# Optimization experiments

Hardware: AMD Instinct MI355X
Metric: run time of the kernel (lower is better)

## Reference

```python
import jax, jax.numpy as jnp
import numpy as np

B, SEQ, HORIZON, NKEYS = 256, 512, 32, 8192
L1, HIDDEN, L2 = 64, 128, 64


def _lstm_layer(x, Wih, Whh, bih, bhh):
    # x: [B, T, IN]; PyTorch gate order i, f, g, o
    Bn, T, _ = x.shape
    H = Whh.shape[1]
    xT = jnp.transpose(x, (1, 0, 2))  # [T, B, IN]
    pre_x = jnp.einsum('tbi,gi->tbg', xT, Wih) + bih + bhh  # precompute input part

    def step(carry, px):
        h, c = carry
        gates = px + h @ Whh.T
        i, f, g, o = jnp.split(gates, 4, axis=-1)
        i = jax.nn.sigmoid(i); f = jax.nn.sigmoid(f)
        g = jnp.tanh(g); o = jax.nn.sigmoid(o)
        c = f * c + i * g
        h = o * jnp.tanh(c)
        return (h, c), h

    h0 = jnp.zeros((Bn, H), x.dtype)
    c0 = jnp.zeros((Bn, H), x.dtype)
    _, hs = jax.lax.scan(step, (h0, c0), pre_x)
    return jnp.transpose(hs, (1, 0, 2))  # [B, T, H]


def setup_inputs():
    key = jax.random.key(0)
    ks = jax.random.split(key, 20)
    s = 0.05
    inp = jax.random.normal(ks[0], (B, SEQ), jnp.float32)
    akey = jax.random.normal(ks[1], (NKEYS, SEQ), jnp.float32)
    aval = jax.random.normal(ks[2], (NKEYS, SEQ + HORIZON), jnp.float32)
    W1 = jax.random.normal(ks[3], (L1, HORIZON + 1), jnp.float32) * s
    b1 = jnp.zeros((L1,), jnp.float32)
    Wih0 = jax.random.normal(ks[4], (4 * HIDDEN, L1), jnp.float32) * s
    Whh0 = jax.random.normal(ks[5], (4 * HIDDEN, HIDDEN), jnp.float32) * s
    bih0 = jnp.zeros((4 * HIDDEN,), jnp.float32)
    bhh0 = jnp.zeros((4 * HIDDEN,), jnp.float32)
    Wih1 = jax.random.normal(ks[6], (4 * HIDDEN, HIDDEN), jnp.float32) * s
    Whh1 = jax.random.normal(ks[7], (4 * HIDDEN, HIDDEN), jnp.float32) * s
    bih1 = jnp.zeros((4 * HIDDEN,), jnp.float32)
    bhh1 = jnp.zeros((4 * HIDDEN,), jnp.float32)
    W2 = jax.random.normal(ks[8], (L2, HIDDEN), jnp.float32) * s
    b2 = jnp.zeros((L2,), jnp.float32)
    W3 = jax.random.normal(ks[9], (HORIZON, L2), jnp.float32) * s
    b3 = jnp.zeros((HORIZON,), jnp.float32)
    return {"input": inp, "attention_key": akey, "attention_value": aval,
            "W1": W1, "b1": b1,
            "Wih0": Wih0, "Whh0": Whh0, "bih0": bih0, "bhh0": bhh0,
            "Wih1": Wih1, "Whh1": Whh1, "bih1": bih1, "bhh1": bhh1,
            "W2": W2, "b2": b2, "W3": W3, "b3": b3}


def reference(input, attention_key, attention_value, W1, b1,
              Wih0, Whh0, bih0, bhh0, Wih1, Whh1, bih1, bhh1,
              W2, b2, W3, b3):
    Bn = input.shape[0]
    # masked distance softmax attention: zero out per-row argmax before softmax
    distance = input @ attention_key.T  # [B, NKEYS]
    max_idx = jnp.argmax(distance, axis=1)
    distance = distance.at[jnp.arange(Bn), max_idx].set(0.0)
    a = jax.nn.softmax(distance, axis=1)
    hist = a @ attention_value  # [B, SEQ + HORIZON]
    # vectorized sliding-window unfold: [B, SEQ, HORIZON]
    win = jnp.arange(SEQ)[:, None] + jnp.arange(HORIZON)[None, :]
    ref_feats = hist[:, win]
    x = jnp.concatenate([input[:, :, None], ref_feats], axis=2)  # [B, SEQ, HORIZON+1]
    x = jnp.tanh(x @ W1.T + b1)  # [B, SEQ, L1]
    h = _lstm_layer(x, Wih0, Whh0, bih0, bhh0)
    h = _lstm_layer(h, Wih1, Whh1, bih1, bhh1)
    h = jnp.tanh(h)
    last = h[:, -1, :]  # [B, HIDDEN]
    l2 = jnp.tanh(last @ W2.T + b2)
    return l2 @ W3.T + b3  # [B, HORIZON]
```

## Files before the change

kernel.cpp:

```cpp
#include <hip/hip_runtime.h>

typedef _Float16 h8 __attribute__((ext_vector_type(8)));
typedef _Float16 h4 __attribute__((ext_vector_type(4)));
typedef float f32x4 __attribute__((ext_vector_type(4)));

__device__ __forceinline__ float fsigm(float x) {
    return __builtin_amdgcn_rcpf(1.0f + __expf(-x));
}
__device__ __forceinline__ float ftanh(float x) {
    return 1.0f - 2.0f * __builtin_amdgcn_rcpf(1.0f + __expf(2.0f * x));
}
__device__ __forceinline__ float fexp2(float x) {
    return __builtin_amdgcn_exp2f(x);
}
__device__ __forceinline__ void lds_barrier() {
    asm volatile("s_waitcnt lgkmcnt(0)\n\ts_barrier" ::: "memory");
}

#define L2E  1.4426950408889634f
#define L2E2 2.8853900817779268f

__global__ __launch_bounds__(256) void k_distM(const float* __restrict__ A,
                                               const float* __restrict__ Bm,
                                               float* __restrict__ C) {
    __shared__ _Float16 Ah[64][40], Al[64][40];
    __shared__ _Float16 Bh[64][40], Bl[64][40];
    const int n0 = blockIdx.x * 64;
    const int m0 = blockIdx.y * 64;
    const int tid = threadIdx.x;
    const int lane = tid & 63, wv = tid >> 6;
    const int quad = lane >> 4, l15 = lane & 15;
    f32x4 acc[4];
#pragma unroll
    for (int i = 0; i < 4; ++i) acc[i] = (f32x4){0.f, 0.f, 0.f, 0.f};

    int sm_[2], skq_[2];
    size_t arow[2], brow[2];
#pragma unroll
    for (int r = 0; r < 2; ++r) {
        int idx = tid + 256 * r;
        sm_[r] = idx >> 3; skq_[r] = (idx & 7) * 4;
        arow[r] = (size_t)(m0 + sm_[r]) * 512 + skq_[r];
        brow[r] = (size_t)(n0 + sm_[r]) * 512 + skq_[r];
    }
    float4 va[2], vb[2];
#pragma unroll
    for (int r = 0; r < 2; ++r) {
        va[r] = *(const float4*)&A[arow[r]];
        vb[r] = *(const float4*)&Bm[brow[r]];
    }

    for (int kt = 0; kt < 512; kt += 32) {
        lds_barrier();
#pragma unroll
        for (int r = 0; r < 2; ++r) {
            float e[4] = {va[r].x, va[r].y, va[r].z, va[r].w};
            h4 hi, lo;
#pragma unroll
            for (int j = 0; j < 4; ++j) {
                _Float16 h = (_Float16)e[j];
                hi[j] = h; lo[j] = (_Float16)(e[j] - (float)h);
            }
            *(h4*)&Ah[sm_[r]][skq_[r]] = hi;
            *(h4*)&Al[sm_[r]][skq_[r]] = lo;
            float f[4] = {vb[r].x, vb[r].y, vb[r].z, vb[r].w};
#pragma unroll
            for (int j = 0; j < 4; ++j) {
                _Float16 h = (_Float16)f[j];
                hi[j] = h; lo[j] = (_Float16)(f[j] - (float)h);
            }
            *(h4*)&Bh[sm_[r]][skq_[r]] = hi;
            *(h4*)&Bl[sm_[r]][skq_[r]] = lo;
        }
        lds_barrier();
        if (kt + 32 < 512) {
#pragma unroll
            for (int r = 0; r < 2; ++r) {
                va[r] = *(const float4*)&A[arow[r] + kt + 32];
                vb[r] = *(const float4*)&Bm[brow[r] + kt + 32];
            }
        }
        h8 ah = *(const h8*)&Ah[wv * 16 + l15][quad * 8];
        h8 al = *(const h8*)&Al[wv * 16 + l15][quad * 8];
#pragma unroll
        for (int nt = 0; nt < 4; ++nt) {
            h8 bhf = *(const h8*)&Bh[nt * 16 + l15][quad * 8];
            h8 blf = *(const h8*)&Bl[nt * 16 + l15][quad * 8];
            acc[nt] = __builtin_amdgcn_mfma_f32_16x16x32_f16(ah, bhf, acc[nt], 0, 0, 0);
            acc[nt] = __builtin_amdgcn_mfma_f32_16x16x32_f16(al, bhf, acc[nt], 0, 0, 0);
            acc[nt] = __builtin_amdgcn_mfma_f32_16x16x32_f16(ah, blf, acc[nt], 0, 0, 0);
        }
    }
#pragma unroll
    for (int nt = 0; nt < 4; ++nt)
#pragma unroll
        for (int r = 0; r < 4; ++r)
            C[(size_t)(m0 + wv * 16 + quad * 4 + r) * 8192 + n0 + nt * 16 + l15] = acc[nt][r];
}

__global__ __launch_bounds__(512) void k_softmax(float* __restrict__ D) {
    __shared__ float row[8192];
    __shared__ float r1[512];
    __shared__ int   ri[512];
    __shared__ float r2[512];
    const int b = blockIdx.x, tid = threadIdx.x;
    float* dr = D + (size_t)b * 8192;
    for (int i = tid; i < 2048; i += 512)
        *(float4*)&row[i * 4] = *(const float4*)&dr[i * 4];
    __syncthreads();

    float m1 = -INFINITY, m2 = -INFINITY; int i1 = 0x7fffffff;
    for (int i = tid; i < 8192; i += 512) {
        float v = row[i];
        if (v > m1) { m2 = m1; m1 = v; i1 = i; }
        else        { m2 = fmaxf(m2, v); }
    }
    r1[tid] = m1; ri[tid] = i1; r2[tid] = m2;
    __syncthreads();
    for (int s = 256; s > 0; s >>= 1) {
        if (tid < s) {
            float am1 = r1[tid], bm1 = r1[tid + s];
            int   ai1 = ri[tid], bi1 = ri[tid + s];
            float am2 = r2[tid], bm2 = r2[tid + s];
            bool bwins = (bm1 > am1) || (bm1 == am1 && bi1 < ai1);
            float wm1 = bwins ? bm1 : am1;
            int   wi1 = bwins ? bi1 : ai1;
            float lm1 = bwins ? am1 : bm1;
            float wm2 = fmaxf(fmaxf(am2, bm2), lm1);
            r1[tid] = wm1; ri[tid] = wi1; r2[tid] = wm2;
        }
        __syncthreads();
    }
    const int   I1 = ri[0];
    const float M  = fmaxf(r2[0], 0.0f);
    __syncthreads();

    float ssum = 0.0f;
    for (int i = tid; i < 8192; i += 512) {
        float v = (i == I1) ? 0.0f : row[i];
        float e = __expf(v - M);
        row[i] = e;
        ssum += e;
    }
    r1[tid] = ssum;
    __syncthreads();
    for (int s = 256; s > 0; s >>= 1) {
        if (tid < s) r1[tid] += r1[tid + s];
        __syncthreads();
    }
    const float inv = 1.0f / r1[0];
    for (int i = tid; i < 2048; i += 512) {
        float4 v = *(float4*)&row[i * 4];
        v.x *= inv; v.y *= inv; v.z *= inv; v.w *= inv;
        *(float4*)&dr[i * 4] = v;
    }
}

__global__ __launch_bounds__(256) void k_histM(const float* __restrict__ A,
                                               const float* __restrict__ Bm,
                                               float* __restrict__ C) {
    __shared__ _Float16 Ah[64][40], Al[64][40];
    __shared__ _Float16 Bh[64][40], Bl[64][40];
    const int n0 = blockIdx.x * 64;
    const int m0 = blockIdx.y * 64;
    const int kz = blockIdx.z;
    const int tid = threadIdx.x;
    const int lane = tid & 63, wv = tid >> 6;
    const int quad = lane >> 4, l15 = lane & 15;
    const int bn = tid & 63;
    const int ko = (tid >> 6) * 8;
    const bool bok = (n0 + bn) < 544;
    f32x4 acc[4];
#pragma unroll
    for (int i = 0; i < 4; ++i) acc[i] = (f32x4){0.f, 0.f, 0.f, 0.f};

    const int k_lo = kz * 512, k_hi = k_lo + 512;
    for (int kt = k_lo; kt < k_hi; kt += 32) {
        __syncthreads();
#pragma unroll
        for (int r = 0; r < 2; ++r) {
            int idx = tid + 256 * r;
            int m = idx >> 3, kq = (idx & 7) * 4;
            float4 v = *(const float4*)&A[(size_t)(m0 + m) * 8192 + kt + kq];
            float e[4] = {v.x, v.y, v.z, v.w};
            h4 hi, lo;
#pragma unroll
            for (int j = 0; j < 4; ++j) {
                _Float16 h = (_Float16)e[j];
                hi[j] = h; lo[j] = (_Float16)(e[j] - (float)h);
            }
            *(h4*)&Ah[m][kq] = hi;
            *(h4*)&Al[m][kq] = lo;
        }
        {
            float e[8];
#pragma unroll
            for (int j = 0; j < 8; ++j)
                e[j] = bok ? Bm[(size_t)(kt + ko + j) * 544 + n0 + bn] : 0.f;
            h8 hi, lo;
#pragma unroll
            for (int j = 0; j < 8; ++j) {
                _Float16 h = (_Float16)e[j];
                hi[j] = h; lo[j] = (_Float16)(e[j] - (float)h);
            }
            *(h8*)&Bh[bn][ko] = hi;
            *(h8*)&Bl[bn][ko] = lo;
        }
        __syncthreads();
        h8 ah = *(const h8*)&Ah[wv * 16 + l15][quad * 8];
        h8 al = *(const h8*)&Al[wv * 16 + l15][quad * 8];
#pragma unroll
        for (int nt = 0; nt < 4; ++nt) {
            h8 bhf = *(const h8*)&Bh[nt * 16 + l15][quad * 8];
            h8 blf = *(const h8*)&Bl[nt * 16 + l15][quad * 8];
            acc[nt] = __builtin_amdgcn_mfma_f32_16x16x32_f16(ah, bhf, acc[nt], 0, 0, 0);
            acc[nt] = __builtin_amdgcn_mfma_f32_16x16x32_f16(al, bhf, acc[nt], 0, 0, 0);
            acc[nt] = __builtin_amdgcn_mfma_f32_16x16x32_f16(ah, blf, acc[nt], 0, 0, 0);
        }
    }
#pragma unroll
    for (int nt = 0; nt < 4; ++nt)
#pragma unroll
        for (int r = 0; r < 4; ++r) {
            int n = n0 + nt * 16 + l15;
            if (n < 544)
                atomicAdd(&C[(size_t)(m0 + wv * 16 + quad * 4 + r) * 544 + n], acc[nt][r]);
        }
}

__global__ __launch_bounds__(256) void k_xfeat(const float* __restrict__ inp,
                                               const float* __restrict__ hist,
                                               const float* __restrict__ W1,
                                               const float* __restrict__ b1,
                                               float* __restrict__ X) {
    __shared__ float w[33 * 64];
    __shared__ float bl[64];
    __shared__ float il[128];
    __shared__ float hl[160];
    const int t0 = blockIdx.x * 128;
    const int b  = blockIdx.y;
    const int tid = threadIdx.x;
    for (int idx = tid; idx < 2112; idx += 256) {
        int o = idx / 33, k = idx % 33;
        w[k * 64 + o] = W1[idx];
    }
    if (tid < 64) bl[tid] = b1[tid];
    if (tid < 128) il[tid] = inp[(size_t)b * 512 + t0 + tid];
    for (int i = tid; i < 159; i += 256) hl[i] = hist[(size_t)b * 544 + t0 + i];
    __syncthreads();
    const int o = tid & 63, tq = tid >> 6;
    for (int it = 0; it < 32; ++it) {
        int tl = it * 4 + tq;
        float acc = fmaf(il[tl], w[o], bl[o]);
#pragma unroll
        for (int j = 0; j < 32; ++j)
            acc = fmaf(hl[tl + j], w[(1 + j) * 64 + o], acc);
        X[(size_t)(b * 512 + t0 + tl) * 64 + o] = ftanh(acc);
    }
}

template <int K>
__device__ __forceinline__ void pregemm_mfma(const float* __restrict__ A,
                                             const float* __restrict__ Bw,
                                             const float* __restrict__ bih,
                                             const float* __restrict__ bhh,
                                             float* __restrict__ C,
                                             int t0, int tcs, int gb, float* sm) {
    _Float16* Ah = (_Float16*)sm;
    _Float16* Al = Ah + 128 * 40;
    _Float16* Bh = Al + 128 * 40;
    _Float16* Bl = Bh + 128 * 40;
    const int n0 = (gb & 3) * 128;
    const int m0 = (gb >> 2) * 128;
    const int tid = threadIdx.x;
    const int lane = tid & 63, wv = tid >> 6;
    const int quad = lane >> 4, l15 = lane & 15;
    const int tcm = (1 << tcs) - 1;
    const int lr0 = tid >> 3, lr1 = lr0 + 64;
    const int kq  = (tid & 7) * 4;
    const int gr0 = m0 + lr0, gr1 = m0 + lr1;
    const size_t ar0 = ((size_t)(gr0 >> tcs) * 512 + t0 + (gr0 & tcm)) * K;
    const size_t ar1 = ((size_t)(gr1 >> tcs) * 512 + t0 + (gr1 & tcm)) * K;
    const size_t br0 = (size_t)(n0 + lr0) * K;
    const size_t br1 = (size_t)(n0 + lr1) * K;
    const float sb0 = (((n0 + lr0) >> 7) == 2) ? L2E2 : L2E;
    const float sb1 = (((n0 + lr1) >> 7) == 2) ? L2E2 : L2E;

    f32x4 acc[8];
#pragma unroll
    for (int i = 0; i < 8; ++i) acc[i] = (f32x4){0.f, 0.f, 0.f, 0.f};

    float4 va0 = *(const float4*)&A[ar0 + kq];
    float4 va1 = *(const float4*)&A[ar1 + kq];
    float4 vb0 = *(const float4*)&Bw[br0 + kq];
    float4 vb1 = *(const float4*)&Bw[br1 + kq];

    for (int kt = 0; kt < K; kt += 32) {
        lds_barrier();
        {
            float e[4]; h4 hi, lo;
            e[0] = va0.x; e[1] = va0.y; e[2] = va0.z; e[3] = va0.w;
#pragma unroll
            for (int j = 0; j < 4; ++j) {
                _Float16 h = (_Float16)e[j];
                hi[j] = h; lo[j] = (_Float16)(e[j] - (float)h);
            }
            *(h4*)&Ah[lr0 * 40 + kq] = hi; *(h4*)&Al[lr0 * 40 + kq] = lo;
            e[0] = va1.x; e[1] = va1.y; e[2] = va1.z; e[3] = va1.w;
#pragma unroll
            for (int j = 0; j < 4; ++j) {
                _Float16 h = (_Float16)e[j];
                hi[j] = h; lo[j] = (_Float16)(e[j] - (float)h);
            }
            *(h4*)&Ah[lr1 * 40 + kq] = hi; *(h4*)&Al[lr1 * 40 + kq] = lo;
            e[0] = vb0.x * sb0; e[1] = vb0.y * sb0; e[2] = vb0.z * sb0; e[3] = vb0.w * sb0;
#pragma unroll
            for (int j = 0; j < 4; ++j) {
                _Float16 h = (_Float16)e[j];
                hi[j] = h; lo[j] = (_Float16)(e[j] - (float)h);
            }
            *(h4*)&Bh[lr0 * 40 + kq] = hi; *(h4*)&Bl[lr0 * 40 + kq] = lo;
            e[0] = vb1.x * sb1; e[1] = vb1.y * sb1; e[2] = vb1.z * sb1; e[3] = vb1.w * sb1;
#pragma unroll
            for (int j = 0; j < 4; ++j) {
                _Float16 h = (_Float16)e[j];
                hi[j] = h; lo[j] = (_Float16)(e[j] - (float)h);
            }
            *(h4*)&Bh[lr1 * 40 + kq] = hi; *(h4*)&Bl[lr1 * 40 + kq] = lo;
        }
        lds_barrier();
        if (kt + 32 < K) {
            va0 = *(const float4*)&A[ar0 + kt + 32 + kq];
            va1 = *(const float4*)&A[ar1 + kt + 32 + kq];
            vb0 = *(const float4*)&Bw[br0 + kt + 32 + kq];
            vb1 = *(const float4*)&Bw[br1 + kt + 32 + kq];
        }
        h8 ah = *(const h8*)&Ah[(wv * 16 + l15) * 40 + quad * 8];
        h8 al = *(const h8*)&Al[(wv * 16 + l15) * 40 + quad * 8];
#pragma unroll
        for (int nt = 0; nt < 8; ++nt) {
            h8 bhf = *(const h8*)&Bh[(nt * 16 + l15) * 40 + quad * 8];
            h8 blf = *(const h8*)&Bl[(nt * 16 + l15) * 40 + quad * 8];
            acc[nt] = __builtin_amdgcn_mfma_f32_16x16x32_f16(ah, bhf, acc[nt], 0, 0, 0);
            acc[nt] = __builtin_amdgcn_mfma_f32_16x16x32_f16(al, bhf, acc[nt], 0, 0, 0);
            acc[nt] = __builtin_amdgcn_mfma_f32_16x16x32_f16(ah, blf, acc[nt], 0, 0, 0);
        }
    }
#pragma unroll
    for (int nt = 0; nt < 8; ++nt) {
        const int n = n0 + nt * 16 + l15;
        const float sc = ((n >> 7) == 2) ? L2E2 : L2E;
        const float bb = (bih[n] + bhh[n]) * sc;
#pragma unroll
        for (int r = 0; r < 4; ++r)
            C[(size_t)(m0 + wv * 16 + quad * 4 + r) * 512 + n] = acc[nt][r] + bb;
    }
}

__device__ __forceinline__ _Float16* hpl(float* sm, int buf, int b) {
    return (_Float16*)sm + ((buf * 16 + b) * 136);
}

template <int PH>
__device__ __forceinline__ void rec_step(
        float* sm,
        const h8 (&wh)[4][4],
        f32x4 (&pcs)[4][4],
        const float*& pp,
        float*& hob, bool wr, bool last,
        float (&c)[4],
        float* __restrict__ Sh, float* __restrict__ Sc,
        int l15, int quad, int un) {
    constexpr int RB = PH & 1;
    const _Float16* hp = hpl(sm, RB, l15);
    h8 hf[4];
#pragma unroll
    for (int q = 0; q < 4; ++q)
        hf[q] = *(const h8*)&hp[q * 32 + quad * 8];

    f32x4 aH[4];
#pragma unroll
    for (int g = 0; g < 4; ++g)
        aH[g] = __builtin_amdgcn_mfma_f32_16x16x32_f16(wh[g][0], hf[0], pcs[PH][g], 0, 0, 0);
#pragma unroll
    for (int g = 0; g < 4; ++g)
        pcs[PH][g] = *(const f32x4*)(pp + g * 128);
    pp += 512;
#pragma unroll
    for (int q = 1; q < 4; ++q)
#pragma unroll
        for (int g = 0; g < 4; ++g)
            aH[g] = __builtin_amdgcn_mfma_f32_16x16x32_f16(wh[g][q], hf[q], aH[g], 0, 0, 0);

    f32x4 hv;
#pragma unroll
    for (int r = 0; r < 4; ++r) {
        float A = fexp2(-aH[0][r]);
        float B = fexp2(-aH[1][r]);
        float Cv = fexp2(aH[2][r]);
        float D = fexp2(-aH[3][r]);
        float fv = __builtin_amdgcn_rcpf(1.0f + B);
        float ig = (Cv - 1.0f) *
                   __builtin_amdgcn_rcpf((1.0f + Cv) * (1.0f + A));
        c[r] = fmaf(c[r], fv, ig);
        float E = fexp2(c[r] * L2E2);
        hv[r] = (E - 1.0f) *
                __builtin_amdgcn_rcpf((1.0f + E) * (1.0f + D));
    }
    h4 hh;
#pragma unroll
    for (int j = 0; j < 4; ++j) hh[j] = (_Float16)hv[j];
    *(h4*)&hpl(sm, 1 - RB, l15)[un] = hh;
    if (wr) {
        *(f32x4*)hob = hv;
        hob += 128;
    }
    if (last) {
        *(f32x4*)Sh = hv;
        f32x4 cv = {c[0], c[1], c[2], c[3]};
        *(f32x4*)Sc = cv;
    }
    lds_barrier();
}

__device__ __forceinline__ void rec_body(const float* __restrict__ P,
                                         const float* __restrict__ Whh,
                                         float* __restrict__ S,
                                         float* __restrict__ Hout,
                                         int t0, int TC, int blk, float* sm) {
    const int b0   = blk * 16;
    const int tid  = threadIdx.x;
    const int lane = tid & 63;
    const int wv   = tid >> 6;
    const int quad = lane >> 4;
    const int l15  = lane & 15;
    const int un   = wv * 16 + quad * 4;
    const int nrow = wv * 16 + l15;

    h8 wh[4][4];
    const float gs[4] = {L2E, L2E, L2E2, L2E};
#pragma unroll
    for (int g = 0; g < 4; ++g) {
        const float sc = gs[g];
        int n = g * 128 + nrow;
#pragma unroll
        for (int q = 0; q < 4; ++q) {
            int kb = q * 32 + quad * 8;
            const float* wp = &Whh[(size_t)n * 128 + kb];
            float4 w0 = *(const float4*)wp;
            float4 w1 = *(const float4*)(wp + 4);
            float we[8] = {w0.x, w0.y, w0.z, w0.w, w1.x, w1.y, w1.z, w1.w};
#pragma unroll
            for (int j = 0; j < 8; ++j)
                wh[g][q][j] = (_Float16)(we[j] * sc);
        }
    }

    float* Sh = S + (size_t)(b0 + l15) * 128 + un;
    float* Sc = Sh + 32768;
    float4 h0 = *(const float4*)Sh;
    float4 c0 = *(const float4*)Sc;
    float c[4] = {c0.x, c0.y, c0.z, c0.w};
    {
        h4 hh;
        hh[0] = (_Float16)h0.x; hh[1] = (_Float16)h0.y;
        hh[2] = (_Float16)h0.z; hh[3] = (_Float16)h0.w;
        *(h4*)&hpl(sm, 0, l15)[un] = hh;
    }

    const bool wr = (Hout != nullptr);
    float* hob = wr ? (Hout + ((size_t)(b0 + l15) * 512 + t0) * 128 + un) : nullptr;

    const float* pp = P + (size_t)(b0 + l15) * TC * 512 + un;
    f32x4 pcs[4][4];
#pragma unroll
    for (int ph = 0; ph < 4; ++ph)
#pragma unroll
        for (int g = 0; g < 4; ++g)
            pcs[ph][g] = *(const f32x4*)(pp + ph * 512 + g * 128);
    pp += 4 * 512;

    lds_barrier();

    for (int tl = 0; tl < TC; tl += 4) {
        rec_step<0>(sm, wh, pcs, pp, hob, wr, false, c, Sh, Sc, l15, quad, un);
        rec_step<1>(sm, wh, pcs, pp, hob, wr, false, c, Sh, Sc, l15, quad, un);
        rec_step<2>(sm, wh, pcs, pp, hob, wr, false, c, Sh, Sc, l15, quad, un);
        rec_step<3>(sm, wh, pcs, pp, hob, wr, (tl + 4 == TC), c, Sh, Sc, l15, quad, un);
    }
}

__global__ __launch_bounds__(512, 1) void k_fused(
        const float* __restrict__ X,    const float* __restrict__ H0,
        const float* __restrict__ Wih0, const float* __restrict__ Wih1,
        const float* __restrict__ bih0, const float* __restrict__ bhh0,
        const float* __restrict__ bih1, const float* __restrict__ bhh1,
        const float* __restrict__ Whh0, const float* __restrict__ Whh1,
        const float* __restrict__ P0r, float* __restrict__ P0w,
        const float* __restrict__ P1r, float* __restrict__ P1w,
        float* __restrict__ S0, float* __restrict__ S1, float* __restrict__ H0out,
        int tr0, int tr1, int tp0, int tp1,
        int v_rec0, int v_rec1, int v_pre0, int v_pre1,
        int TC, int tcs) {
    __shared__ float smem[20480];
    const int bid = blockIdx.x;
    if (bid < 16) {
        if (v_rec0) rec_body(P0r, Whh0, S0, H0out, tr0, TC, bid, smem);
        return;
    }
    if (bid < 32) {
        if (v_rec1) rec_body(P1r, Whh1, S1, nullptr, tr1, TC, bid - 16, smem);
        return;
    }
    int gb = bid - 32;
    const int npre = 8 * TC;
    if (gb < npre) {
        if (v_pre0) pregemm_mfma<64>(X, Wih0, bih0, bhh0, P0w, tp0, tcs, gb, smem);
        return;
    }
    gb -= npre;
    if (v_pre1) pregemm_mfma<128>(H0, Wih1, bih1, bhh1, P1w, tp1, tcs, gb, smem);
}

__global__ __launch_bounds__(64) void k_tail(const float* __restrict__ Hs,
                                             const float* __restrict__ W2,
                                             const float* __restrict__ b2,
                                             const float* __restrict__ W3,
                                             const float* __restrict__ b3,
                                             float* __restrict__ out) {
    __shared__ float last[128], l2s[64];
    const int b = blockIdx.x, tid = threadIdx.x;
    last[tid]      = ftanh(Hs[(size_t)b * 128 + tid]);
    last[tid + 64] = ftanh(Hs[(size_t)b * 128 + 64 + tid]);
    __syncthreads();
    float acc = b2[tid];
#pragma unroll 4
    for (int j = 0; j < 128; ++j) acc = fmaf(W2[(size_t)tid * 128 + j], last[j], acc);
    l2s[tid] = ftanh(acc);
    __syncthreads();
    if (tid < 32) {
        float a2 = b3[tid];
#pragma unroll 4
        for (int o = 0; o < 64; ++o) a2 = fmaf(W3[(size_t)tid * 64 + o], l2s[o], a2);
        out[(size_t)b * 32 + tid] = a2;
    }
}

extern "C" void kernel_launch(void* const* d_in, const int* in_sizes, int n_in,
                              void* d_out, int out_size, void* d_ws, size_t ws_size,
                              hipStream_t stream) {
    (void)in_sizes; (void)n_in; (void)out_size;
    const float* inp  = (const float*)d_in[0];
    const float* akey = (const float*)d_in[1];
    const float* aval = (const float*)d_in[2];
    const float* W1   = (const float*)d_in[3];
    const float* b1   = (const float*)d_in[4];
    const float* Wih0 = (const float*)d_in[5];
    const float* Whh0 = (const float*)d_in[6];
    const float* bih0 = (const float*)d_in[7];
    const float* bhh0 = (const float*)d_in[8];
    const float* Wih1 = (const float*)d_in[9];
    const float* Whh1 = (const float*)d_in[10];
    const float* bih1 = (const float*)d_in[11];
    const float* bhh1 = (const float*)d_in[12];
    const float* W2   = (const float*)d_in[13];
    const float* b2   = (const float*)d_in[14];
    const float* W3   = (const float*)d_in[15];
    const float* b3   = (const float*)d_in[16];

    float* ws   = (float*)d_ws;
    float* dist = ws;
    float* hist = dist + 2097152;
    float* X    = hist + 139264;
    float* S0   = X + 8388672;
    float* S1   = S0 + 65536;
    float* H0   = S1 + 65536;
    float* PB   = H0 + 16777216;
    const size_t fixed = (size_t)(PB - ws);

    int TC = 16, tcs = 4;
    if ((fixed + 4ull * ((size_t)256 * 32 * 512 + 2048)) * 4 <= ws_size) { TC = 32; tcs = 5; }
    const size_t pchunk = (size_t)256 * TC * 512 + 2048;
    float* P0b[2] = {PB, PB + pchunk};
    float* P1b[2] = {PB + 2 * pchunk, PB + 3 * pchunk};

    k_distM<<<dim3(128, 4), 256, 0, stream>>>(inp, akey, dist);
    k_softmax<<<256, 512, 0, stream>>>(dist);
    hipMemsetAsync(hist, 0, 139264 * 4, stream);
    k_histM<<<dim3(9, 4, 16), 256, 0, stream>>>(dist, aval, hist);
    k_xfeat<<<dim3(4, 256), 256, 0, stream>>>(inp, hist, W1, b1, X);
    hipMemsetAsync(S0, 0, (size_t)2 * 65536 * 4, stream);

    const int NC = 512 / TC;
    const int nblocks = 32 + 16 * TC;
    for (int k = -1; k <= NC + 1; ++k) {
        int v_rec0 = (k >= 0 && k < NC);
        int v_rec1 = (k >= 2 && k < NC + 2);
        int v_pre0 = (k + 1 >= 0 && k + 1 < NC);
        int v_pre1 = (k - 1 >= 0 && k - 1 < NC);
        if (!(v_rec0 | v_rec1 | v_pre0 | v_pre1)) continue;
        const float* P0r = P0b[k & 1];
        float*       P0w = P0b[(k + 1) & 1];
        const float* P1r = P1b[k & 1];
        float*       P1w = P1b[(k + 1) & 1];
        k_fused<<<nblocks, 512, 0, stream>>>(
            X, H0, Wih0, Wih1, bih0, bhh0, bih1, bhh1, Whh0, Whh1,
            P0r, P0w, P1r, P1w, S0, S1, H0,
            k * TC, (k - 2) * TC, (k + 1) * TC, (k - 1) * TC,
            v_rec0, v_rec1, v_pre0, v_pre1, TC, tcs);
    }
    k_tail<<<256, 64, 0, stream>>>(S1, W2, b2, W3, b3, (float*)d_out);
}
```

Baseline: 988.6 us.

## Replace per-chunk kernel launches with a persistent cooperative kernel using grid sync

The LSTM pipeline previously launched one fused kernel per time chunk and reloaded recurrent weights and h/c state from global memory on each launch. It now launches a single cooperative kernel of 256 blocks that keeps Whh in registers and the cell state across chunks, and separates chunks with grid-wide syncs. The pre-GEMM work is spread over the remaining 224 blocks with a strided loop. This removes launch overhead and state round-trips, at the cost of grid barriers and fewer blocks for the input projection when TC is large.

```diff
diff --git a/kernel.cpp b/kernel.cpp
--- a/kernel.cpp
+++ b/kernel.cpp
@@ -1,12 +1,12 @@
 #include <hip/hip_runtime.h>
+#include <hip/hip_cooperative_groups.h>
+
+namespace cg = cooperative_groups;
 
 typedef _Float16 h8 __attribute__((ext_vector_type(8)));
 typedef _Float16 h4 __attribute__((ext_vector_type(4)));
 typedef float f32x4 __attribute__((ext_vector_type(4)));
 
-__device__ __forceinline__ float fsigm(float x) {
-    return __builtin_amdgcn_rcpf(1.0f + __expf(-x));
-}
 __device__ __forceinline__ float ftanh(float x) {
     return 1.0f - 2.0f * __builtin_amdgcn_rcpf(1.0f + __expf(2.0f * x));
 }
@@ -423,21 +423,10 @@
     lds_barrier();
 }
 
-__device__ __forceinline__ void rec_body(const float* __restrict__ P,
-                                         const float* __restrict__ Whh,
-                                         float* __restrict__ S,
-                                         float* __restrict__ Hout,
-                                         int t0, int TC, int blk, float* sm) {
-    const int b0   = blk * 16;
-    const int tid  = threadIdx.x;
-    const int lane = tid & 63;
-    const int wv   = tid >> 6;
-    const int quad = lane >> 4;
-    const int l15  = lane & 15;
-    const int un   = wv * 16 + quad * 4;
-    const int nrow = wv * 16 + l15;
-
-    h8 wh[4][4];
+__device__ __forceinline__ void rec_init(const float* __restrict__ Whh,
+                                         h8 (&wh)[4][4], float (&c)[4],
+                                         float* sm, int l15, int quad,
+                                         int un, int nrow) {
     const float gs[4] = {L2E, L2E, L2E2, L2E};
 #pragma unroll
     for (int g = 0; g < 4; ++g) {
@@ -455,21 +444,24 @@
                 wh[g][q][j] = (_Float16)(we[j] * sc);
         }
     }
-
-    float* Sh = S + (size_t)(b0 + l15) * 128 + un;
-    float* Sc = Sh + 32768;
-    float4 h0 = *(const float4*)Sh;
-    float4 c0 = *(const float4*)Sc;
-    float c[4] = {c0.x, c0.y, c0.z, c0.w};
-    {
-        h4 hh;
-        hh[0] = (_Float16)h0.x; hh[1] = (_Float16)h0.y;
-        hh[2] = (_Float16)h0.z; hh[3] = (_Float16)h0.w;
-        *(h4*)&hpl(sm, 0, l15)[un] = hh;
-    }
-
+#pragma unroll
+    for (int r = 0; r < 4; ++r) c[r] = 0.0f;
+    h4 z = (h4){(_Float16)0.f, (_Float16)0.f, (_Float16)0.f, (_Float16)0.f};
+    *(h4*)&hpl(sm, 0, l15)[un] = z;
+    lds_barrier();
+}
+
+__device__ __forceinline__ void rec_chunk(const float* __restrict__ P,
+                                          float* __restrict__ Hout,
+                                          float* __restrict__ S1l,
+                                          int t0, int TC,
+                                          const h8 (&wh)[4][4], float (&c)[4],
+                                          float* sm, int b0, int l15, int quad, int un) {
     const bool wr = (Hout != nullptr);
     float* hob = wr ? (Hout + ((size_t)(b0 + l15) * 512 + t0) * 128 + un) : nullptr;
+    const bool dolast = (S1l != nullptr);
+    float* Sh = dolast ? (S1l + (size_t)(b0 + l15) * 128 + un) : (float*)nullptr;
+    float* Sc = dolast ? (Sh + 32768) : (float*)nullptr;
 
     const float* pp = P + (size_t)(b0 + l15) * TC * 512 + un;
     f32x4 pcs[4][4];
@@ -479,47 +471,78 @@
         for (int g = 0; g < 4; ++g)
             pcs[ph][g] = *(const f32x4*)(pp + ph * 512 + g * 128);
     pp += 4 * 512;
-
-    lds_barrier();
 
     for (int tl = 0; tl < TC; tl += 4) {
         rec_step<0>(sm, wh, pcs, pp, hob, wr, false, c, Sh, Sc, l15, quad, un);
         rec_step<1>(sm, wh, pcs, pp, hob, wr, false, c, Sh, Sc, l15, quad, un);
         rec_step<2>(sm, wh, pcs, pp, hob, wr, false, c, Sh, Sc, l15, quad, un);
-        rec_step<3>(sm, wh, pcs, pp, hob, wr, (tl + 4 == TC), c, Sh, Sc, l15, quad, un);
-    }
-}
-
-__global__ __launch_bounds__(512, 1) void k_fused(
-        const float* __restrict__ X,    const float* __restrict__ H0,
+        rec_step<3>(sm, wh, pcs, pp, hob, wr, dolast && (tl + 4 == TC),
+                    c, Sh, Sc, l15, quad, un);
+    }
+}
+
+__global__ __launch_bounds__(512, 1) void k_persist(
+        const float* __restrict__ X,    float* __restrict__ H0,
         const float* __restrict__ Wih0, const float* __restrict__ Wih1,
         const float* __restrict__ bih0, const float* __restrict__ bhh0,
         const float* __restrict__ bih1, const float* __restrict__ bhh1,
         const float* __restrict__ Whh0, const float* __restrict__ Whh1,
-        const float* __restrict__ P0r, float* __restrict__ P0w,
-        const float* __restrict__ P1r, float* __restrict__ P1w,
-        float* __restrict__ S0, float* __restrict__ S1, float* __restrict__ H0out,
-        int tr0, int tr1, int tp0, int tp1,
-        int v_rec0, int v_rec1, int v_pre0, int v_pre1,
-        int TC, int tcs) {
+        float* __restrict__ P0a, float* __restrict__ P0b,
+        float* __restrict__ P1a, float* __restrict__ P1b,
+        float* __restrict__ S1,
+        int TC, int tcs, int NC) {
+    cg::grid_group gg = cg::this_grid();
     __shared__ float smem[20480];
     const int bid = blockIdx.x;
-    if (bid < 16) {
-        if (v_rec0) rec_body(P0r, Whh0, S0, H0out, tr0, TC, bid, smem);
-        return;
-    }
+    const int tid = threadIdx.x;
+
+    h8 wh[4][4];
+    float c[4];
+    int b0 = 0, l15 = 0, quad = 0, un = 0;
     if (bid < 32) {
-        if (v_rec1) rec_body(P1r, Whh1, S1, nullptr, tr1, TC, bid - 16, smem);
-        return;
-    }
-    int gb = bid - 32;
-    const int npre = 8 * TC;
-    if (gb < npre) {
-        if (v_pre0) pregemm_mfma<64>(X, Wih0, bih0, bhh0, P0w, tp0, tcs, gb, smem);
-        return;
-    }
-    gb -= npre;
-    if (v_pre1) pregemm_mfma<128>(H0, Wih1, bih1, bhh1, P1w, tp1, tcs, gb, smem);
+        const int lane = tid & 63, wv = tid >> 6;
+        quad = lane >> 4; l15 = lane & 15;
+        un = wv * 16 + quad * 4;
+        const int nrow = wv * 16 + l15;
+        b0 = (bid & 15) * 16;
+        rec_init(bid < 16 ? Whh0 : Whh1, wh, c, smem, l15, quad, un, nrow);
+    }
+
+    for (int k = -1; k <= NC + 1; ++k) {
+        gg.sync();
+        const bool v_rec0 = (k >= 0 && k < NC);
+        const bool v_rec1 = (k >= 2 && k < NC + 2);
+        const bool v_pre0 = (k + 1 >= 0 && k + 1 < NC);
+        const bool v_pre1 = (k - 1 >= 0 && k - 1 < NC);
+        if (bid < 16) {
+            if (v_rec0) {
+                const float* P0r = (k & 1) ? P0b : P0a;
+                rec_chunk(P0r, H0, nullptr, k * TC, TC, wh, c, smem,
+                          b0, l15, quad, un);
+            }
+        } else if (bid < 32) {
+            if (v_rec1) {
+                const int kk = k - 2;
+                const float* P1r = (k & 1) ? P1b : P1a;
+                rec_chunk(P1r, nullptr, (kk == NC - 1) ? S1 : nullptr,
+                          kk * TC, TC, wh, c, smem, b0, l15, quad, un);
+            }
+        } else {
+            const int w = bid - 32;
+            if (v_pre0) {
+                float* P0w = ((k + 1) & 1) ? P0b : P0a;
+                for (int t = w; t < 8 * TC; t += 224)
+                    pregemm_mfma<64>(X, Wih0, bih0, bhh0, P0w,
+                                     (k + 1) * TC, tcs, t, smem);
+            }
+            if (v_pre1) {
+                float* P1w = ((k + 1) & 1) ? P1b : P1a;
+                for (int t = w; t < 8 * TC; t += 224)
+                    pregemm_mfma<128>(H0, Wih1, bih1, bhh1, P1w,
+                                      (k - 1) * TC, tcs, t, smem);
+            }
+        }
+    }
 }
 
 __global__ __launch_bounds__(64) void k_tail(const float* __restrict__ Hs,
@@ -580,34 +603,32 @@
 
     int TC = 16, tcs = 4;
     if ((fixed + 4ull * ((size_t)256 * 32 * 512 + 2048)) * 4 <= ws_size) { TC = 32; tcs = 5; }
+    int NC = 512 / TC;
     const size_t pchunk = (size_t)256 * TC * 512 + 2048;
-    float* P0b[2] = {PB, PB + pchunk};
-    float* P1b[2] = {PB + 2 * pchunk, PB + 3 * pchunk};
+    float* p0a = PB;
+    float* p0b = PB + pchunk;
+    float* p1a = PB + 2 * pchunk;
+    float* p1b = PB + 3 * pchunk;
 
     k_distM<<<dim3(128, 4), 256, 0, stream>>>(inp, akey, dist);
     k_softmax<<<256, 512, 0, stream>>>(dist);
-    hipMemsetAsync(hist, 0, 139264 * 4, stream);
+    (void)hipMemsetAsync(hist, 0, 139264 * 4, stream);
     k_histM<<<dim3(9, 4, 16), 256, 0, stream>>>(dist, aval, hist);
     k_xfeat<<<dim3(4, 256), 256, 0, stream>>>(inp, hist, W1, b1, X);
-    hipMemsetAsync(S0, 0, (size_t)2 * 65536 * 4, stream);
-
-    const int NC = 512 / TC;
-    const int nblocks = 32 + 16 * TC;
-    for (int k = -1; k <= NC + 1; ++k) {
-        int v_rec0 = (k >= 0 && k < NC);
-        int v_rec1 = (k >= 2 && k < NC + 2);
-        int v_pre0 = (k + 1 >= 0 && k + 1 < NC);
-        int v_pre1 = (k - 1 >= 0 && k - 1 < NC);
-        if (!(v_rec0 | v_rec1 | v_pre0 | v_pre1)) continue;
-        const float* P0r = P0b[k & 1];
-        float*       P0w = P0b[(k + 1) & 1];
-        const float* P1r = P1b[k & 1];
-        float*       P1w = P1b[(k + 1) & 1];
-        k_fused<<<nblocks, 512, 0, stream>>>(
-            X, H0, Wih0, Wih1, bih0, bhh0, bih1, bhh1, Whh0, Whh1,
-            P0r, P0w, P1r, P1w, S0, S1, H0,
-            k * TC, (k - 2) * TC, (k + 1) * TC, (k - 1) * TC,
-            v_rec0, v_rec1, v_pre0, v_pre1, TC, tcs);
-    }
+
+    void* kargs[] = {
+        (void*)&X,    (void*)&H0,
+        (void*)&Wih0, (void*)&Wih1,
+        (void*)&bih0, (void*)&bhh0,
+        (void*)&bih1, (void*)&bhh1,
+        (void*)&Whh0, (void*)&Whh1,
+        (void*)&p0a,  (void*)&p0b,
+        (void*)&p1a,  (void*)&p1b,
+        (void*)&S1,
+        (void*)&TC,   (void*)&tcs, (void*)&NC,
+    };
+    (void)hipLaunchCooperativeKernel((void*)k_persist, dim3(256), dim3(512),
+                                     kargs, 0, stream);
+
     k_tail<<<256, 64, 0, stream>>>(S1, W2, b2, W3, b3, (float*)d_out);
 }
```

Measured after the change: 1.468 ms. 1.49x slower.
